# Kernel optimization log

Measured on AMD Instinct MI355X. Metric: run time of the kernel, lower is better.

The kernel has to match this reference:

```python
import jax, jax.numpy as jnp
from jax import lax
import numpy as np

B, CIN, COUT, H, W = 8, 64, 64, 128, 128
K = 3
KK = K * K  # 9 kernel taps


def setup_inputs() -> dict:
    key = jax.random.key(0)
    ks = jax.random.split(key, 10)
    n = jax.random.normal
    s = 0.05  # keep activations in a sane range
    return {
        "Fi": n(ks[0], (B, CIN, H, W), jnp.float32),
        "Fe": n(ks[1], (B, CIN, H, W), jnp.float32),
        "w1": n(ks[2], (CIN, 2 * CIN, 5, 5), jnp.float32) * s,
        "b1": n(ks[3], (CIN,), jnp.float32) * s,
        "w2": n(ks[4], (CIN, CIN, 3, 3), jnp.float32) * s,
        "b2": n(ks[5], (CIN,), jnp.float32) * s,
        "w_off": n(ks[6], (3 * KK, CIN, 3, 3), jnp.float32) * s,
        "b_off": n(ks[7], (3 * KK,), jnp.float32) * s,
        "w_dcn": n(ks[8], (COUT, CIN, 3, 3), jnp.float32) * s,
        "b_dcn": n(ks[9], (COUT,), jnp.float32) * s,
    }


def _conv(x, w, b, pad):
    y = lax.conv_general_dilated(x, w, (1, 1), [(pad, pad), (pad, pad)],
                                 dimension_numbers=('NCHW', 'OIHW', 'NCHW'))
    return y + b[None, :, None, None]


def _leaky(x):
    return jnp.where(x >= 0, x, 0.1 * x)  # LeakyReLU(0.1)


def _bilinear(img, y, x):
    # img [B,C,H,W]; y, x [B,KK,H,W] fractional sampling coords; zero padding OOB
    Bn, C, Hi, Wi = img.shape
    y0 = jnp.floor(y)
    x0 = jnp.floor(x)
    flat = img.reshape(Bn, C, Hi * Wi)
    out = jnp.zeros((Bn, C) + y.shape[1:], img.dtype)
    for dy, dx in ((0, 0), (0, 1), (1, 0), (1, 1)):
        yi = y0 + dy
        xi = x0 + dx
        wgt = (1.0 - jnp.abs(y - yi)) * (1.0 - jnp.abs(x - xi))
        valid = (yi >= 0) & (yi <= Hi - 1) & (xi >= 0) & (xi <= Wi - 1)
        yc = jnp.clip(yi, 0, Hi - 1).astype(jnp.int32)
        xc = jnp.clip(xi, 0, Wi - 1).astype(jnp.int32)
        idx = (yc * Wi + xc).reshape(Bn, 1, -1)
        v = jnp.take_along_axis(flat, jnp.broadcast_to(idx, (Bn, C, idx.shape[-1])), axis=2)
        v = v.reshape(Bn, C, *y.shape[1:])  # [B,C,KK,H,W]
        out = out + v * (wgt * valid)[:, None]
    return out


def _dcn(x, feat, w_off, b_off, w, b):
    # modulated deformable conv (DCNv2), k=3, stride=1, pad=1, dilation=1
    oo = _conv(feat, w_off, b_off, 1)                 # [B, 3*KK, H, W]
    o1, o2, m = jnp.split(oo, 3, axis=1)              # dy, dx, mask logits
    offset_out = jnp.concatenate([o1, o2], axis=1)
    mask = jax.nn.sigmoid(m)                          # [B,KK,H,W]
    ky, kx = jnp.meshgrid(jnp.arange(K), jnp.arange(K), indexing='ij')
    ky = ky.reshape(KK)
    kx = kx.reshape(KK)
    base_y = (jnp.arange(H)[None, :, None] - 1 + ky[:, None, None]).astype(x.dtype)  # [KK,H,1]
    base_x = (jnp.arange(W)[None, None, :] - 1 + kx[:, None, None]).astype(x.dtype)  # [KK,1,W]
    ys = base_y[None] + o1                            # [B,KK,H,W]
    xs = base_x[None] + o2                            # [B,KK,H,W]
    samp = _bilinear(x, ys, xs) * mask[:, None]       # [B,C,KK,H,W]
    out = jnp.einsum('bckhw,ock->bohw', samp, w.reshape(w.shape[0], w.shape[1], KK))
    return offset_out, out + b[None, :, None, None]


def reference(Fi, Fe, w1, b1, w2, b2, w_off, b_off, w_dcn, b_dcn):
    feat = _leaky(_conv(jnp.concatenate([Fi, Fe], axis=1), w1, b1, 2))
    feat = _leaky(_conv(feat, w2, b2, 1))
    offset_out, aligned = _dcn(Fe, feat, w_off, b_off, w_dcn, b_dcn)
    Ff = jnp.concatenate([Fi, aligned], axis=1)
    return offset_out, Ff
```

## Files before the change

kernel.cpp:

```cpp
#include <hip/hip_runtime.h>
#include <hip/hip_bf16.h>

typedef __bf16 bf16_t;
typedef __attribute__((ext_vector_type(8))) __bf16 bf16x8;
typedef __attribute__((ext_vector_type(4))) float f32x4;

#define Bn 8
#define Hh 128
#define Ww 128
#define HW 16384

#define WP1_B   ((size_t)0)
#define WP2_B   ((size_t)409600)
#define WPO_B   ((size_t)483328)
#define WDCN_B  ((size_t)520192)
#define BIAS_B  ((size_t)667648)
#define XT_B    ((size_t)668672)
#define F1_B    (XT_B + 33554432)
#define F2_B    (F1_B + 16777216)

__global__ void prep_kernel(const float* __restrict__ w1, const float* __restrict__ w2,
                            const float* __restrict__ woff, const float* __restrict__ wdcn,
                            const float* __restrict__ b1, const float* __restrict__ b2,
                            const float* __restrict__ boff, const float* __restrict__ bdcn,
                            char* __restrict__ wsb) {
    bf16_t* wp1 = (bf16_t*)(wsb + WP1_B);
    bf16_t* wp2 = (bf16_t*)(wsb + WP2_B);
    bf16_t* wpo = (bf16_t*)(wsb + WPO_B);
    bf16_t* wd  = (bf16_t*)(wsb + WDCN_B);
    float*  bias= (float*)(wsb + BIAS_B);
    int tid = blockIdx.x * blockDim.x + threadIdx.x;
    int nt  = gridDim.x * blockDim.x;
    for (int i = tid; i < 25*4*4*64*8; i += nt) {
        int j = i & 7, q = i >> 3;
        int n = q % 64; q /= 64;
        int g = q & 3;  q >>= 2;
        int ck = q & 3; int t = q >> 2;
        int cin = ck*32 + g*8 + j;
        wp1[i] = (bf16_t)w1[(n*128 + cin)*25 + t];
    }
    for (int i = tid; i < 9*2*4*64*8; i += nt) {
        int j = i & 7, q = i >> 3;
        int n = q % 64; q /= 64;
        int g = q & 3;  q >>= 2;
        int ck = q & 1; int t = q >> 1;
        int cin = ck*32 + g*8 + j;
        wp2[i] = (bf16_t)w2[(n*64 + cin)*9 + t];
    }
    for (int i = tid; i < 9*2*4*32*8; i += nt) {
        int j = i & 7, q = i >> 3;
        int n = q & 31; q >>= 5;
        int g = q & 3;  q >>= 2;
        int ck = q & 1; int t = q >> 1;
        int cin = ck*32 + g*8 + j;
        wpo[i] = (n < 27) ? (bf16_t)woff[(n*64 + cin)*9 + t] : (bf16_t)0.f;
    }
    for (int i = tid; i < 18*4*4*16*8; i += nt) {
        int j = i & 7, f = i >> 3;
        int l15 = f & 15; f >>= 4;
        int l4  = f & 3;  f >>= 2;
        int ntl = f & 3;  int kc = f >> 2;
        int kg = kc*32 + l4*8 + j;
        int tap = kg >> 6, c = kg & 63;
        int n = ntl*16 + l15;
        wd[i] = (bf16_t)wdcn[n*576 + c*9 + tap];
    }
    if (tid < 64) { bias[tid] = b1[tid]; bias[64+tid] = b2[tid]; bias[160+tid] = bdcn[tid]; }
    if (tid >= 64 && tid < 96) { int n = tid - 64; bias[128+n] = (n < 27) ? boff[n] : 0.f; }
}

__global__ __launch_bounds__(256) void nhwc_kernel(const float* __restrict__ Fi,
                                                   const float* __restrict__ Fe,
                                                   bf16_t* __restrict__ Xt) {
    __shared__ bf16_t tile[64][136];
    const int b  = blockIdx.y;
    const int p0 = blockIdx.x * 64;
    const int px = threadIdx.x & 63;
    const int csub = threadIdx.x >> 6;
    for (int ci = 0; ci < 32; ++ci) {
        int c = csub * 32 + ci;
        const float* src = (c < 64) ? (Fi + (((size_t)(b*64 + c)) << 14))
                                    : (Fe + (((size_t)(b*64 + (c-64))) << 14));
        tile[px][c] = (bf16_t)src[p0 + px];
    }
    __syncthreads();
    const int px2 = threadIdx.x >> 2;
    const int cc  = (threadIdx.x & 3) * 32;
    bf16x8* dst = (bf16x8*)(Xt + ((size_t)(b*HW) + p0 + px2) * 128 + cc);
    const bf16x8* srcl = (const bf16x8*)(&tile[px2][cc]);
    dst[0] = srcl[0]; dst[1] = srcl[1]; dst[2] = srcl[2]; dst[3] = srcl[3];
}

template <int CIN_, int KS, int WM, int WN, bool LEAKY, int COUTP, bool OUTF32, bool OFFS>
__global__ __launch_bounds__(256) void conv_mfma(const bf16_t* __restrict__ Xt,
                                                 const bf16_t* __restrict__ Wp,
                                                 const float* __restrict__ bias,
                                                 bf16_t* __restrict__ outb,
                                                 float* __restrict__ outf,
                                                 float* __restrict__ out0) {
    constexpr int PAD = KS / 2;
    constexpr int HR  = WM + KS - 1;
    constexpr int HC  = 32 + KS - 1;
    constexpr int NC  = CIN_ / 32;
    __shared__ bf16_t stg[HR * HC * 40];

    const int tid  = threadIdx.x;
    const int lane = tid & 63;
    const int wid  = tid >> 6;
    const int wm   = wid / WN;
    const int wn   = wid % WN;
    const int b    = blockIdx.z;
    const int h0   = blockIdx.y * WM;
    const int w0   = blockIdx.x * 32;
    const int l15  = lane & 15;
    const int l4   = lane >> 4;

    f32x4 acc[2][2];
#pragma unroll
    for (int i = 0; i < 2; ++i)
#pragma unroll
        for (int j = 0; j < 2; ++j)
#pragma unroll
            for (int r = 0; r < 4; ++r) acc[i][j][r] = 0.f;

    const int site = tid;
    const int srow = site / HC, scol = site % HC;
    const int gh = h0 - PAD + srow, gw = w0 - PAD + scol;
    const bool active = site < HR * HC;
    const bool inb = active && ((unsigned)gh < 128u) && ((unsigned)gw < 128u);
    const bf16_t Z0 = (bf16_t)0.f;
    const bf16x8 zv = {Z0, Z0, Z0, Z0, Z0, Z0, Z0, Z0};

    const bf16x8* wpt = (const bf16x8*)Wp;

    for (int ck = 0; ck < NC; ++ck) {
        if (active) {
            bf16x8 v0 = zv, v1 = zv, v2 = zv, v3 = zv;
            if (inb) {
                const bf16x8* gp = (const bf16x8*)(Xt + (((size_t)(b*HW) + (gh << 7) + gw)) * CIN_ + ck * 32);
                v0 = gp[0]; v1 = gp[1]; v2 = gp[2]; v3 = gp[3];
            }
            bf16x8* ldst = (bf16x8*)(&stg[site * 40]);
            ldst[0] = v0; ldst[1] = v1; ldst[2] = v2; ldst[3] = v3;
        }
        __syncthreads();
        int t = 0;
#pragma unroll
        for (int dy = 0; dy < KS; ++dy) {
#pragma unroll
            for (int dx = 0; dx < KS; ++dx, ++t) {
                bf16x8 a0 = *(const bf16x8*)(&stg[((wm + dy) * HC + (l15 + dx)) * 40 + l4 * 8]);
                bf16x8 a1 = *(const bf16x8*)(&stg[((wm + dy) * HC + (16 + l15 + dx)) * 40 + l4 * 8]);
                const bf16x8* wb = wpt + ((size_t)((t * NC + ck) * 4 + l4)) * COUTP + wn * 32 + l15;
                bf16x8 b0 = wb[0];
                bf16x8 b1 = wb[16];
                acc[0][0] = __builtin_amdgcn_mfma_f32_16x16x32_bf16(a0, b0, acc[0][0], 0, 0, 0);
                acc[0][1] = __builtin_amdgcn_mfma_f32_16x16x32_bf16(a0, b1, acc[0][1], 0, 0, 0);
                acc[1][0] = __builtin_amdgcn_mfma_f32_16x16x32_bf16(a1, b0, acc[1][0], 0, 0, 0);
                acc[1][1] = __builtin_amdgcn_mfma_f32_16x16x32_bf16(a1, b1, acc[1][1], 0, 0, 0);
            }
        }
        __syncthreads();
    }

    const int hrow = h0 + wm;
#pragma unroll
    for (int mh = 0; mh < 2; ++mh) {
#pragma unroll
        for (int nh = 0; nh < 2; ++nh) {
            const int n = wn * 32 + nh * 16 + l15;
            const float bs = bias[n];
#pragma unroll
            for (int r = 0; r < 4; ++r) {
                const int px = w0 + mh * 16 + l4 * 4 + r;
                float v = acc[mh][nh][r] + bs;
                if (LEAKY) v = (v >= 0.f) ? v : 0.1f * v;
                const size_t pix = (size_t)(hrow << 7) + px;
                if (OUTF32) outf[(((size_t)(b * COUTP + n)) << 14) + pix] = v;
                else        outb[(((size_t)(b * HW)) + pix) * COUTP + n] = (bf16_t)v;
                if (OFFS) {
                    if (n < 18) out0[(((size_t)(b * 18 + n)) << 14) + pix] = v;
                }
            }
        }
    }
}

__global__ void copy_fi(const float* __restrict__ Fi, float* __restrict__ out1) {
    const int b = blockIdx.y;
    const int i = blockIdx.x * blockDim.x + threadIdx.x;
    const int e = i << 2;
    const int c = e >> 14;
    const int p = e & 16383;
    const float4* src = reinterpret_cast<const float4*>(Fi);
    float4* dst = reinterpret_cast<float4*>(out1);
    size_t se = ((size_t)b << 20) + e;
    size_t de = (((size_t)(b * 128 + c)) << 14) + p;
    dst[de >> 2] = src[se >> 2];
}

__global__ __launch_bounds__(512) void dcn_mfma(const bf16_t* __restrict__ Xt,
                                                const float* __restrict__ OO,
                                                const bf16_t* __restrict__ Wd,
                                                const float* __restrict__ bias,
                                                float* __restrict__ out1) {
    __shared__ bf16_t Bs[10 * 4 * 4 * 16 * 8];

    const int tid  = threadIdx.x;
    const int lane = tid & 63;
    const int wave = tid >> 6;
    const int l15  = lane & 15;
    const int l4   = lane >> 4;
    const int b    = blockIdx.y;
    const int p0   = blockIdx.x * 256 + wave * 32;

    f32x4 acc[2][4];
#pragma unroll
    for (int nt = 0; nt < 4; ++nt) {
        const float bs = bias[nt * 16 + l15];
#pragma unroll
        for (int a = 0; a < 2; ++a) { acc[a][nt][0] = bs; acc[a][nt][1] = bs; acc[a][nt][2] = bs; acc[a][nt][3] = bs; }
    }

    const bf16_t* feb = Xt + ((size_t)(b * HW)) * 128 + 64;
    const bf16x8* Bsv = (const bf16x8*)Bs;
    const bf16x8* Wdv = (const bf16x8*)Wd;

#pragma unroll
    for (int phase = 0; phase < 2; ++phase) {
        const int fbase = phase * 2560;
        const int fcnt  = phase ? 2048 : 2560;
        bf16x8* Bsw = (bf16x8*)Bs;
        for (int f = tid; f < fcnt; f += 512) Bsw[f] = Wdv[fbase + f];
        __syncthreads();

        const int t0 = phase ? 5 : 0;
        const int t1 = phase ? 9 : 5;
        for (int k = t0; k < t1; ++k) {
            const int ky = k / 3, kx = k % 3;
#pragma unroll
            for (int a = 0; a < 2; ++a) {
                const int p  = p0 + a * 16 + l15;
                const int h  = p >> 7, w = p & 127;
                const float o1v = OO[(((size_t)(b * 32 + k)) << 14) + p];
                const float o2v = OO[(((size_t)(b * 32 + 9 + k)) << 14) + p];
                const float ml  = OO[(((size_t)(b * 32 + 18 + k)) << 14) + p];
                const float m = 1.f / (1.f + __expf(-ml));

                const float y = (float)(h - 1 + ky) + o1v;
                const float x = (float)(w - 1 + kx) + o2v;
                const float y0f = floorf(y), x0f = floorf(x);
                const float fy = y - y0f, fx = x - x0f;
                const int y0 = (int)y0f, x0 = (int)x0f;

                const bool vy0 = (unsigned)y0 < 128u;
                const bool vy1 = (unsigned)(y0 + 1) < 128u;
                const bool vx0 = (unsigned)x0 < 128u;
                const bool vx1 = (unsigned)(x0 + 1) < 128u;

                const int y0c = min(max(y0, 0), 127);
                const int y1c = min(max(y0 + 1, 0), 127);
                const int x0c = min(max(x0, 0), 127);
                const int x1c = min(max(x0 + 1, 0), 127);

                float w00 = (1.f - fy) * (1.f - fx) * m; w00 = (vy0 && vx0) ? w00 : 0.f;
                float w01 = (1.f - fy) * fx * m;         w01 = (vy0 && vx1) ? w01 : 0.f;
                float w10 = fy * (1.f - fx) * m;         w10 = (vy1 && vx0) ? w10 : 0.f;
                float w11 = fy * fx * m;                 w11 = (vy1 && vx1) ? w11 : 0.f;

                const bf16_t* p00 = feb + ((size_t)((y0c << 7) + x0c)) * 128;
                const bf16_t* p01 = feb + ((size_t)((y0c << 7) + x1c)) * 128;
                const bf16_t* p10 = feb + ((size_t)((y1c << 7) + x0c)) * 128;
                const bf16_t* p11 = feb + ((size_t)((y1c << 7) + x1c)) * 128;

#pragma unroll
                for (int cc = 0; cc < 2; ++cc) {
                    const int c0 = cc * 32 + l4 * 8;
                    const bf16x8 v00 = *(const bf16x8*)(p00 + c0);
                    const bf16x8 v01 = *(const bf16x8*)(p01 + c0);
                    const bf16x8 v10 = *(const bf16x8*)(p10 + c0);
                    const bf16x8 v11 = *(const bf16x8*)(p11 + c0);
                    bf16x8 af;
#pragma unroll
                    for (int j = 0; j < 8; ++j) {
                        af[j] = (bf16_t)(w00 * (float)v00[j] + w01 * (float)v01[j]
                                       + w10 * (float)v10[j] + w11 * (float)v11[j]);
                    }
                    const int kcl = (k * 2 + cc) - phase * 10;
#pragma unroll
                    for (int nt = 0; nt < 4; ++nt) {
                        const bf16x8 bf = Bsv[((kcl * 4 + nt) * 4 + l4) * 16 + l15];
                        acc[a][nt] = __builtin_amdgcn_mfma_f32_16x16x32_bf16(af, bf, acc[a][nt], 0, 0, 0);
                    }
                }
            }
        }
        __syncthreads();
    }

#pragma unroll
    for (int a = 0; a < 2; ++a) {
#pragma unroll
        for (int nt = 0; nt < 4; ++nt) {
            const int o = nt * 16 + l15;
#pragma unroll
            for (int r = 0; r < 4; ++r) {
                const int p = p0 + a * 16 + l4 * 4 + r;
                out1[(((size_t)(b * 128 + 64 + o)) << 14) + p] = acc[a][nt][r];
            }
        }
    }
}

extern "C" void kernel_launch(void* const* d_in, const int* in_sizes, int n_in,
                              void* d_out, int out_size, void* d_ws, size_t ws_size,
                              hipStream_t stream) {
    const float* Fi    = (const float*)d_in[0];
    const float* Fe    = (const float*)d_in[1];
    const float* w1    = (const float*)d_in[2];
    const float* b1    = (const float*)d_in[3];
    const float* w2    = (const float*)d_in[4];
    const float* b2    = (const float*)d_in[5];
    const float* w_off = (const float*)d_in[6];
    const float* b_off = (const float*)d_in[7];
    const float* w_dcn = (const float*)d_in[8];
    const float* b_dcn = (const float*)d_in[9];

    char* wsb = (char*)d_ws;
    bf16_t* wp1   = (bf16_t*)(wsb + WP1_B);
    bf16_t* wp2   = (bf16_t*)(wsb + WP2_B);
    bf16_t* wpo   = (bf16_t*)(wsb + WPO_B);
    bf16_t* wdcnf = (bf16_t*)(wsb + WDCN_B);
    float*  bias  = (float*)(wsb + BIAS_B);
    bf16_t* Xt    = (bf16_t*)(wsb + XT_B);
    bf16_t* feat1 = (bf16_t*)(wsb + F1_B);
    bf16_t* feat2 = (bf16_t*)(wsb + F2_B);
    float*  OO    = (float*)(wsb + F1_B);

    float* out0 = (float*)d_out;
    float* out1 = out0 + (size_t)Bn * 18 * HW;

    prep_kernel<<<256, 256, 0, stream>>>(w1, w2, w_off, w_dcn, b1, b2, b_off, b_dcn, wsb);

    nhwc_kernel<<<dim3(256, 8), 256, 0, stream>>>(Fi, Fe, Xt);

    conv_mfma<128, 5, 2, 2, true, 64, false, false>
        <<<dim3(4, 64, 8), 256, 0, stream>>>(Xt, wp1, bias, feat1, nullptr, nullptr);

    conv_mfma<64, 3, 2, 2, true, 64, false, false>
        <<<dim3(4, 64, 8), 256, 0, stream>>>(feat1, wp2, bias + 64, feat2, nullptr, nullptr);

    conv_mfma<64, 3, 4, 1, false, 32, true, true>
        <<<dim3(4, 32, 8), 256, 0, stream>>>(feat2, wpo, bias + 128, nullptr, OO, out0);

    copy_fi<<<dim3(1024, 8), 256, 0, stream>>>(Fi, out1);

    dcn_mfma<<<dim3(64, 8), 512, 0, stream>>>(Xt, OO, wdcnf, bias + 160, out1);
}
```

Baseline: 354.7 us.

## Enlarge conv tiles to 4x64 pixels with full output channels per wave

Each conv block now covers 4 rows by 64 columns, and each wave computes one row across all output channels (4 M-tiles by COUTP/16 N-tiles). The staging loop strides over the larger halo so all threads help fill shared memory. This cuts the halo overhead per output pixel and reuses each A fragment across more MFMAs and each weight load across more pixels. In exchange it uses more accumulator registers (up to 64 floats), which may lower occupancy, a larger LDS footprint, and fewer blocks in the grid.

```diff
diff --git a/kernel.cpp b/kernel.cpp
--- a/kernel.cpp
+++ b/kernel.cpp
@@ -91,7 +91,7 @@
     dst[0] = srcl[0]; dst[1] = srcl[1]; dst[2] = srcl[2]; dst[3] = srcl[3];
 }
 
-template <int CIN_, int KS, int WM, int WN, bool LEAKY, int COUTP, bool OUTF32, bool OFFS>
+template <int CIN_, int KS, int COUTP, bool LEAKY, bool OUTF32, bool OFFS>
 __global__ __launch_bounds__(256) void conv_mfma(const bf16_t* __restrict__ Xt,
                                                  const bf16_t* __restrict__ Wp,
                                                  const float* __restrict__ bias,
@@ -99,48 +99,43 @@
                                                  float* __restrict__ outf,
                                                  float* __restrict__ out0) {
     constexpr int PAD = KS / 2;
-    constexpr int HR  = WM + KS - 1;
-    constexpr int HC  = 32 + KS - 1;
+    constexpr int HR  = 4 + KS - 1;
+    constexpr int HC  = 64 + KS - 1;
     constexpr int NC  = CIN_ / 32;
+    constexpr int NT  = COUTP / 16;
     __shared__ bf16_t stg[HR * HC * 40];
 
     const int tid  = threadIdx.x;
     const int lane = tid & 63;
     const int wid  = tid >> 6;
-    const int wm   = wid / WN;
-    const int wn   = wid % WN;
     const int b    = blockIdx.z;
-    const int h0   = blockIdx.y * WM;
-    const int w0   = blockIdx.x * 32;
+    const int h0   = blockIdx.y * 4;
+    const int w0   = blockIdx.x * 64;
     const int l15  = lane & 15;
     const int l4   = lane >> 4;
 
-    f32x4 acc[2][2];
-#pragma unroll
-    for (int i = 0; i < 2; ++i)
-#pragma unroll
-        for (int j = 0; j < 2; ++j)
-#pragma unroll
-            for (int r = 0; r < 4; ++r) acc[i][j][r] = 0.f;
-
-    const int site = tid;
-    const int srow = site / HC, scol = site % HC;
-    const int gh = h0 - PAD + srow, gw = w0 - PAD + scol;
-    const bool active = site < HR * HC;
-    const bool inb = active && ((unsigned)gh < 128u) && ((unsigned)gw < 128u);
+    f32x4 acc[4][NT];
+#pragma unroll
+    for (int m = 0; m < 4; ++m)
+#pragma unroll
+        for (int nt = 0; nt < NT; ++nt)
+#pragma unroll
+            for (int r = 0; r < 4; ++r) acc[m][nt][r] = 0.f;
+
     const bf16_t Z0 = (bf16_t)0.f;
     const bf16x8 zv = {Z0, Z0, Z0, Z0, Z0, Z0, Z0, Z0};
-
     const bf16x8* wpt = (const bf16x8*)Wp;
 
     for (int ck = 0; ck < NC; ++ck) {
-        if (active) {
+        for (int s = tid; s < HR * HC; s += 256) {
+            const int srow = s / HC, scol = s % HC;
+            const int gh = h0 - PAD + srow, gw = w0 - PAD + scol;
             bf16x8 v0 = zv, v1 = zv, v2 = zv, v3 = zv;
-            if (inb) {
+            if (((unsigned)gh < 128u) && ((unsigned)gw < 128u)) {
                 const bf16x8* gp = (const bf16x8*)(Xt + (((size_t)(b*HW) + (gh << 7) + gw)) * CIN_ + ck * 32);
                 v0 = gp[0]; v1 = gp[1]; v2 = gp[2]; v3 = gp[3];
             }
-            bf16x8* ldst = (bf16x8*)(&stg[site * 40]);
+            bf16x8* ldst = (bf16x8*)(&stg[s * 40]);
             ldst[0] = v0; ldst[1] = v1; ldst[2] = v2; ldst[3] = v3;
         }
         __syncthreads();
@@ -149,31 +144,35 @@
         for (int dy = 0; dy < KS; ++dy) {
 #pragma unroll
             for (int dx = 0; dx < KS; ++dx, ++t) {
-                bf16x8 a0 = *(const bf16x8*)(&stg[((wm + dy) * HC + (l15 + dx)) * 40 + l4 * 8]);
-                bf16x8 a1 = *(const bf16x8*)(&stg[((wm + dy) * HC + (16 + l15 + dx)) * 40 + l4 * 8]);
-                const bf16x8* wb = wpt + ((size_t)((t * NC + ck) * 4 + l4)) * COUTP + wn * 32 + l15;
-                bf16x8 b0 = wb[0];
-                bf16x8 b1 = wb[16];
-                acc[0][0] = __builtin_amdgcn_mfma_f32_16x16x32_bf16(a0, b0, acc[0][0], 0, 0, 0);
-                acc[0][1] = __builtin_amdgcn_mfma_f32_16x16x32_bf16(a0, b1, acc[0][1], 0, 0, 0);
-                acc[1][0] = __builtin_amdgcn_mfma_f32_16x16x32_bf16(a1, b0, acc[1][0], 0, 0, 0);
-                acc[1][1] = __builtin_amdgcn_mfma_f32_16x16x32_bf16(a1, b1, acc[1][1], 0, 0, 0);
+                bf16x8 a[4];
+#pragma unroll
+                for (int m = 0; m < 4; ++m)
+                    a[m] = *(const bf16x8*)(&stg[((wid + dy) * HC + (m * 16 + l15 + dx)) * 40 + l4 * 8]);
+                bf16x8 bb[NT];
+#pragma unroll
+                for (int nt = 0; nt < NT; ++nt)
+                    bb[nt] = wpt[((size_t)((t * NC + ck) * 4 + l4)) * COUTP + nt * 16 + l15];
+#pragma unroll
+                for (int m = 0; m < 4; ++m)
+#pragma unroll
+                    for (int nt = 0; nt < NT; ++nt)
+                        acc[m][nt] = __builtin_amdgcn_mfma_f32_16x16x32_bf16(a[m], bb[nt], acc[m][nt], 0, 0, 0);
             }
         }
         __syncthreads();
     }
 
-    const int hrow = h0 + wm;
-#pragma unroll
-    for (int mh = 0; mh < 2; ++mh) {
-#pragma unroll
-        for (int nh = 0; nh < 2; ++nh) {
-            const int n = wn * 32 + nh * 16 + l15;
+    const int hrow = h0 + wid;
+#pragma unroll
+    for (int m = 0; m < 4; ++m) {
+#pragma unroll
+        for (int nt = 0; nt < NT; ++nt) {
+            const int n = nt * 16 + l15;
             const float bs = bias[n];
 #pragma unroll
             for (int r = 0; r < 4; ++r) {
-                const int px = w0 + mh * 16 + l4 * 4 + r;
-                float v = acc[mh][nh][r] + bs;
+                const int px = w0 + m * 16 + l4 * 4 + r;
+                float v = acc[m][nt][r] + bs;
                 if (LEAKY) v = (v >= 0.f) ? v : 0.1f * v;
                 const size_t pix = (size_t)(hrow << 7) + px;
                 if (OUTF32) outf[(((size_t)(b * COUTP + n)) << 14) + pix] = v;
@@ -344,14 +343,14 @@
 
     nhwc_kernel<<<dim3(256, 8), 256, 0, stream>>>(Fi, Fe, Xt);
 
-    conv_mfma<128, 5, 2, 2, true, 64, false, false>
-        <<<dim3(4, 64, 8), 256, 0, stream>>>(Xt, wp1, bias, feat1, nullptr, nullptr);
-
-    conv_mfma<64, 3, 2, 2, true, 64, false, false>
-        <<<dim3(4, 64, 8), 256, 0, stream>>>(feat1, wp2, bias + 64, feat2, nullptr, nullptr);
-
-    conv_mfma<64, 3, 4, 1, false, 32, true, true>
-        <<<dim3(4, 32, 8), 256, 0, stream>>>(feat2, wpo, bias + 128, nullptr, OO, out0);
+    conv_mfma<128, 5, 64, true, false, false>
+        <<<dim3(2, 32, 8), 256, 0, stream>>>(Xt, wp1, bias, feat1, nullptr, nullptr);
+
+    conv_mfma<64, 3, 64, true, false, false>
+        <<<dim3(2, 32, 8), 256, 0, stream>>>(feat1, wp2, bias + 64, feat2, nullptr, nullptr);
+
+    conv_mfma<64, 3, 32, false, true, true>
+        <<<dim3(2, 32, 8), 256, 0, stream>>>(feat2, wpo, bias + 128, nullptr, OO, out0);
 
     copy_fi<<<dim3(1024, 8), 256, 0, stream>>>(Fi, out1);
 
```

After: 329.1 us. 7.2% less time.
